# Optimization experiments

Measured on AMD Instinct MI355X. Metric: run time of the kernel, lower is better.

Reference implementation:

```python
import jax, jax.numpy as jnp
import numpy as np
from jax.scipy.stats import norm
from jax.scipy.special import ndtri

B, S, F = 512, 2048, 128

def setup_inputs() -> dict:
    key = jax.random.key(0)
    k1, k2, k3 = jax.random.split(key, 3)
    x = jax.random.normal(k1, (B, F), dtype=jnp.float32)
    cdf_data = jax.random.normal(k2, (S, F), dtype=jnp.float32)
    bw_param = jax.random.uniform(k3, (1, F), dtype=jnp.float32)
    return {"x": x, "cdf_data": cdf_data, "bw_param": bw_param}

def reference(x, cdf_data, bw_param):
    # trainable bandwidths: bw = sigmoid(raw param), shape [1, F]
    bw = jax.nn.sigmoid(bw_param)[0]  # [F]
    # Pairwise Gaussian-CDF KDE: for each (b, f), mean over stored samples s of
    # Phi((x[b,f] - cdf_data[s,f]) / bw[f]).  Intermediate z: [B, S, F].
    z = (x[:, None, :] - cdf_data[None, :, :]) / bw  # [B, S, F]
    u = jnp.mean(norm.cdf(z), axis=1)               # [B, F], uniform-ish in (0,1)
    # normal_backtransform=True: map uniform -> standard normal via inverse CDF
    return ndtri(u)
```

## Files before the change

kernel.cpp:

```cpp
#include <hip/hip_runtime.h>
#include <math.h>

#define FDIM  128
#define SDIM  2048
#define BDIM  512
#define GPTS  128
#define SP    8
#define PARTS 4
#define BLOCK1 (FDIM * PARTS)
#define XMIN  (-6.5)
#define XSPAN (13.0)

__device__ __forceinline__ double ndtri_pair(double u, double cu) {
    double q = u - 0.5;
    if (fabs(q) <= 0.425) {
        double r = 0.180625 - q * q;
        double num = (((((((2.5090809287301226727e3  * r + 3.3430575583588128105e4) * r +
                            6.7265770927008700853e4) * r + 4.5921953931549871457e4) * r +
                            1.3731693765509461125e4) * r + 1.9715909503065514427e3) * r +
                            1.3314166789178437745e2) * r + 3.3871328727963666080e0);
        double den = (((((((5.2264952788528545610e3  * r + 2.8729085735721942674e4) * r +
                            3.9307895800092710610e4) * r + 2.1213794301586595867e4) * r +
                            5.3941960214247511077e3) * r + 6.8718700749205790830e2) * r +
                            4.2313330701600911252e1) * r + 1.0);
        return q * num / den;
    }
    double r = (q < 0.0) ? u : cu;
    r = fmax(r, 1e-300);
    r = sqrt(-log(r));
    double val;
    if (r <= 5.0) {
        r -= 1.6;
        double num = (((((((7.74545014278341407640e-4 * r + 2.27238449892691845833e-2) * r +
                            2.41780725177450611770e-1) * r + 1.27045825245236838258e0) * r +
                            3.64784832476320460504e0)  * r + 5.76949722146069140550e0) * r +
                            4.63033784615654529590e0)  * r + 1.42343711074968357734e0);
        double den = (((((((1.05075007164441684324e-9 * r + 5.47593808499534494600e-4) * r +
                            1.51986665636164571966e-2) * r + 1.48103976427480074590e-1) * r +
                            6.89767334985100004550e-1) * r + 1.67638483018380384940e0) * r +
                            2.05319162663775882187e0)  * r + 1.0);
        val = num / den;
    } else {
        r -= 5.0;
        double num = (((((((2.01033439929228813265e-7 * r + 2.71155556874348757815e-5) * r +
                            1.24266094738807843860e-3) * r + 2.65321895265761230930e-2) * r +
                            2.96560571828504891230e-1) * r + 1.78482653991729133580e0) * r +
                            5.46378491116411436990e0)  * r + 6.65790464350110377720e0);
        double den = (((((((2.04426310338993978564e-15 * r + 1.42151175831644588870e-7) * r +
                            1.84631831751005468180e-5)  * r + 7.86869131145613259100e-4) * r +
                            1.48753612908506148525e-2)  * r + 1.36929880922735805310e-1) * r +
                            5.99832206555887937690e-1)  * r + 1.0);
        val = num / den;
    }
    return (q < 0.0) ? -val : val;
}

__device__ __forceinline__ float half_erfc_ex(float a, float& ex_out) {
    float t  = __builtin_amdgcn_rcpf(fmaf(0.3275911f, a, 1.0f));
    float ex = __expf(-a * a);
    ex_out = ex;
    float q  = fmaf(0.53070271450f, t, -0.72657601350f);
    q        = fmaf(q, t,  0.71070687050f);
    q        = fmaf(q, t, -0.14224836800f);
    q        = fmaf(q, t,  0.12741479600f);
    return q * t * ex;
}

__global__ __launch_bounds__(BLOCK1) void build_kernel(
    const float* __restrict__ cdf, const float* __restrict__ bwp,
    float* __restrict__ accP, float* __restrict__ dacP, int* __restrict__ npP)
{
    const int g    = blockIdx.x >> 3;
    const int sp   = blockIdx.x & (SP - 1);
    const int f    = threadIdx.x & (FDIM - 1);
    const int part = threadIdx.x >> 7;

    const float p = bwp[f];
    const float s = (1.0f + __expf(-p)) * 0.70710678118654752f;
    const float xg = (float)(XMIN + (double)g * (XSPAN / (GPTS - 1)));

    const int chunk = SDIM / SP / PARTS;
    const int base  = sp * (SDIM / SP) + part * chunk;
    const float* cp = cdf + base * FDIM + f;

    float acc0 = 0.f, acc1 = 0.f, acc2 = 0.f, acc3 = 0.f;
    float dac = 0.f;
    int npos = 0;

    for (int i = 0; i < chunk; i += 4) {
        float c0 = cp[0 * FDIM];
        float c1 = cp[1 * FDIM];
        float c2 = cp[2 * FDIM];
        float c3 = cp[3 * FDIM];
        cp += 4 * FDIM;

        float d0 = xg - c0, d1 = xg - c1, d2 = xg - c2, d3 = xg - c3;
        float x0, x1, x2, x3;
        float e0 = half_erfc_ex(fabsf(d0) * s, x0);
        float e1 = half_erfc_ex(fabsf(d1) * s, x1);
        float e2 = half_erfc_ex(fabsf(d2) * s, x2);
        float e3 = half_erfc_ex(fabsf(d3) * s, x3);

        bool p0 = d0 >= 0.f, p1 = d1 >= 0.f, p2 = d2 >= 0.f, p3 = d3 >= 0.f;
        acc0 += p0 ? -e0 : e0;
        acc1 += p1 ? -e1 : e1;
        acc2 += p2 ? -e2 : e2;
        acc3 += p3 ? -e3 : e3;
        npos += (int)p0 + (int)p1 + (int)p2 + (int)p3;
        dac  += (x0 + x1) + (x2 + x3);
    }

    __shared__ float sacc[PARTS][FDIM];
    __shared__ float sdac[PARTS][FDIM];
    __shared__ int   snp[PARTS][FDIM];
    sacc[part][f] = (acc0 + acc1) + (acc2 + acc3);
    sdac[part][f] = dac;
    snp[part][f]  = npos;
    __syncthreads();

    if (part == 0) {
        float a  = (sacc[0][f] + sacc[1][f]) + (sacc[2][f] + sacc[3][f]);
        float da = (sdac[0][f] + sdac[1][f]) + (sdac[2][f] + sdac[3][f]);
        int   np = snp[0][f] + snp[1][f] + snp[2][f] + snp[3][f];
        const int o = blockIdx.x * FDIM + f;
        accP[o] = a;
        dacP[o] = da;
        npP[o]  = np;
    }
}

__global__ __launch_bounds__(256) void table_kernel(
    const float* __restrict__ accP, const float* __restrict__ dacP,
    const int* __restrict__ npP, const float* __restrict__ bwp,
    double* __restrict__ Tu, double* __restrict__ Tcu, double* __restrict__ Td)
{
    const int idx = blockIdx.x * 256 + threadIdx.x;
    const int g = idx >> 7;
    const int f = idx & (FDIM - 1);
    (void)g;

    double a = 0.0, da = 0.0;
    int np = 0;
    #pragma unroll
    for (int sp = 0; sp < SP; ++sp) {
        const int o = ((idx >> 7) * SP + sp) * FDIM + f;
        a  += (double)accP[o];
        da += (double)dacP[o];
        np += npP[o];
    }
    const double invS = 1.0 / (double)SDIM;
    double u  = ((double)np + a) * invS;
    double cu = ((double)(SDIM - np) - a) * invS;
    double invbw = 1.0 + exp(-(double)bwp[f]);
    double du = da * invbw * (1.0 / ((double)SDIM * 2.5066282746310002));
    Tu[idx]  = u;
    Tcu[idx] = cu;
    Td[idx]  = du;
}

__global__ __launch_bounds__(256) void interp_kernel(
    const float* __restrict__ x,
    const double* __restrict__ Tu, const double* __restrict__ Tcu,
    const double* __restrict__ Td, float* __restrict__ out)
{
    const int idx = blockIdx.x * 256 + threadIdx.x;
    const int f = idx & (FDIM - 1);

    const double H = XSPAN / (GPTS - 1);
    double t = ((double)x[idx] - XMIN) * ((GPTS - 1) / XSPAN);
    t = fmin(fmax(t, 0.0), (double)(GPTS - 1));
    int i = (int)t;
    if (i > GPTS - 2) i = GPTS - 2;
    double w = t - (double)i;

    const int o0 = i * FDIM + f;
    const int o1 = o0 + FDIM;
    double u0 = Tu[o0],  u1 = Tu[o1];
    double c0 = Tcu[o0], c1 = Tcu[o1];
    double m0 = Td[o0],  m1 = Td[o1];

    double w2 = w * w, w3 = w2 * w;
    double h00 = 2.0 * w3 - 3.0 * w2 + 1.0;
    double h10 = w3 - 2.0 * w2 + w;
    double h01 = 3.0 * w2 - 2.0 * w3;
    double h11 = w3 - w2;
    double dterm = H * (h10 * m0 + h11 * m1);
    double u  = h00 * u0 + h01 * u1 + dterm;
    double cu = h00 * c0 + h01 * c1 - dterm;

    out[idx] = (float)ndtri_pair(u, cu);
}

extern "C" void kernel_launch(void* const* d_in, const int* in_sizes, int n_in,
                              void* d_out, int out_size, void* d_ws, size_t ws_size,
                              hipStream_t stream) {
    const float* x   = (const float*)d_in[0];
    const float* cdf = (const float*)d_in[1];
    const float* bwp = (const float*)d_in[2];
    float* out = (float*)d_out;

    const size_t GF   = (size_t)GPTS * FDIM;
    const size_t GSPF = (size_t)GPTS * SP * FDIM;
    char* wsb = (char*)d_ws;
    double* Tu   = (double*)wsb;
    double* Tcu  = Tu + GF;
    double* Td   = Tcu + GF;
    float*  accP = (float*)(Td + GF);
    float*  dacP = accP + GSPF;
    int*    npP  = (int*)(dacP + GSPF);

    build_kernel<<<dim3(GPTS * SP), dim3(BLOCK1), 0, stream>>>(cdf, bwp, accP, dacP, npP);
    table_kernel<<<dim3(GF / 256), dim3(256), 0, stream>>>(accP, dacP, npP, bwp, Tu, Tcu, Td);
    interp_kernel<<<dim3((BDIM * FDIM) / 256), dim3(256), 0, stream>>>(x, Tu, Tcu, Td, out);
}
```

Baseline: 80.37 us.

## Halve interpolation grid, fuse table reduction into interp kernel

Cuts the KDE grid from 128 to 64 points over a narrower range and doubles the sample splits per point, so build_kernel does half the erfc evaluations. It removes the separate table kernel by having interp_kernel reduce the 16 partial sums for the two bracketing grid points directly. It also adds an unroll hint to the build loop. The coarser grid and clipped range may reduce the accuracy of the Hermite interpolation, and the fused reduction does redundant gather work for each output element.

```diff
diff --git a/kernel.cpp b/kernel.cpp
--- a/kernel.cpp
+++ b/kernel.cpp
@@ -4,12 +4,12 @@
 #define FDIM  128
 #define SDIM  2048
 #define BDIM  512
-#define GPTS  128
-#define SP    8
+#define GPTS  64
+#define SP    16
 #define PARTS 4
 #define BLOCK1 (FDIM * PARTS)
-#define XMIN  (-6.5)
-#define XSPAN (13.0)
+#define XMIN  (-6.0)
+#define XSPAN (12.0)
 
 __device__ __forceinline__ double ndtri_pair(double u, double cu) {
     double q = u - 0.5;
@@ -70,7 +70,7 @@
     const float* __restrict__ cdf, const float* __restrict__ bwp,
     float* __restrict__ accP, float* __restrict__ dacP, int* __restrict__ npP)
 {
-    const int g    = blockIdx.x >> 3;
+    const int g    = blockIdx.x >> 4;
     const int sp   = blockIdx.x & (SP - 1);
     const int f    = threadIdx.x & (FDIM - 1);
     const int part = threadIdx.x >> 7;
@@ -87,6 +87,7 @@
     float dac = 0.f;
     int npos = 0;
 
+    #pragma unroll 2
     for (int i = 0; i < chunk; i += 4) {
         float c0 = cp[0 * FDIM];
         float c1 = cp[1 * FDIM];
@@ -129,56 +130,46 @@
     }
 }
 
-__global__ __launch_bounds__(256) void table_kernel(
+__global__ __launch_bounds__(256) void interp_kernel(
+    const float* __restrict__ x, const float* __restrict__ bwp,
     const float* __restrict__ accP, const float* __restrict__ dacP,
-    const int* __restrict__ npP, const float* __restrict__ bwp,
-    double* __restrict__ Tu, double* __restrict__ Tcu, double* __restrict__ Td)
-{
-    const int idx = blockIdx.x * 256 + threadIdx.x;
-    const int g = idx >> 7;
-    const int f = idx & (FDIM - 1);
-    (void)g;
-
-    double a = 0.0, da = 0.0;
-    int np = 0;
-    #pragma unroll
-    for (int sp = 0; sp < SP; ++sp) {
-        const int o = ((idx >> 7) * SP + sp) * FDIM + f;
-        a  += (double)accP[o];
-        da += (double)dacP[o];
-        np += npP[o];
-    }
-    const double invS = 1.0 / (double)SDIM;
-    double u  = ((double)np + a) * invS;
-    double cu = ((double)(SDIM - np) - a) * invS;
-    double invbw = 1.0 + exp(-(double)bwp[f]);
-    double du = da * invbw * (1.0 / ((double)SDIM * 2.5066282746310002));
-    Tu[idx]  = u;
-    Tcu[idx] = cu;
-    Td[idx]  = du;
-}
-
-__global__ __launch_bounds__(256) void interp_kernel(
-    const float* __restrict__ x,
-    const double* __restrict__ Tu, const double* __restrict__ Tcu,
-    const double* __restrict__ Td, float* __restrict__ out)
+    const int* __restrict__ npP, float* __restrict__ out)
 {
     const int idx = blockIdx.x * 256 + threadIdx.x;
     const int f = idx & (FDIM - 1);
 
-    const double H = XSPAN / (GPTS - 1);
     double t = ((double)x[idx] - XMIN) * ((GPTS - 1) / XSPAN);
     t = fmin(fmax(t, 0.0), (double)(GPTS - 1));
     int i = (int)t;
     if (i > GPTS - 2) i = GPTS - 2;
     double w = t - (double)i;
 
-    const int o0 = i * FDIM + f;
-    const int o1 = o0 + FDIM;
-    double u0 = Tu[o0],  u1 = Tu[o1];
-    double c0 = Tcu[o0], c1 = Tcu[o1];
-    double m0 = Td[o0],  m1 = Td[o1];
-
+    double a0 = 0.0, da0 = 0.0, a1 = 0.0, da1 = 0.0;
+    int np0 = 0, np1 = 0;
+    const float* pA = accP + (i * SP) * FDIM + f;
+    const float* pD = dacP + (i * SP) * FDIM + f;
+    const int*   pN = npP  + (i * SP) * FDIM + f;
+    #pragma unroll
+    for (int sp = 0; sp < SP; ++sp) {
+        a0  += (double)pA[sp * FDIM];
+        da0 += (double)pD[sp * FDIM];
+        np0 += pN[sp * FDIM];
+        a1  += (double)pA[(SP + sp) * FDIM];
+        da1 += (double)pD[(SP + sp) * FDIM];
+        np1 += pN[(SP + sp) * FDIM];
+    }
+
+    const double invS = 1.0 / (double)SDIM;
+    const double invbw = 1.0 + (double)__expf(-bwp[f]);
+    const double mscale = invbw * (invS / 2.5066282746310002);
+    double u0 = ((double)np0 + a0) * invS;
+    double cu0 = ((double)(SDIM - np0) - a0) * invS;
+    double m0 = da0 * mscale;
+    double u1 = ((double)np1 + a1) * invS;
+    double cu1 = ((double)(SDIM - np1) - a1) * invS;
+    double m1 = da1 * mscale;
+
+    const double H = XSPAN / (GPTS - 1);
     double w2 = w * w, w3 = w2 * w;
     double h00 = 2.0 * w3 - 3.0 * w2 + 1.0;
     double h10 = w3 - 2.0 * w2 + w;
@@ -186,7 +177,7 @@
     double h11 = w3 - w2;
     double dterm = H * (h10 * m0 + h11 * m1);
     double u  = h00 * u0 + h01 * u1 + dterm;
-    double cu = h00 * c0 + h01 * c1 - dterm;
+    double cu = h00 * cu0 + h01 * cu1 - dterm;
 
     out[idx] = (float)ndtri_pair(u, cu);
 }
@@ -199,17 +190,11 @@
     const float* bwp = (const float*)d_in[2];
     float* out = (float*)d_out;
 
-    const size_t GF   = (size_t)GPTS * FDIM;
     const size_t GSPF = (size_t)GPTS * SP * FDIM;
-    char* wsb = (char*)d_ws;
-    double* Tu   = (double*)wsb;
-    double* Tcu  = Tu + GF;
-    double* Td   = Tcu + GF;
-    float*  accP = (float*)(Td + GF);
-    float*  dacP = accP + GSPF;
-    int*    npP  = (int*)(dacP + GSPF);
+    float* accP = (float*)d_ws;
+    float* dacP = accP + GSPF;
+    int*   npP  = (int*)(dacP + GSPF);
 
     build_kernel<<<dim3(GPTS * SP), dim3(BLOCK1), 0, stream>>>(cdf, bwp, accP, dacP, npP);
-    table_kernel<<<dim3(GF / 256), dim3(256), 0, stream>>>(accP, dacP, npP, bwp, Tu, Tcu, Td);
-    interp_kernel<<<dim3((BDIM * FDIM) / 256), dim3(256), 0, stream>>>(x, Tu, Tcu, Td, out);
-}
+    interp_kernel<<<dim3((BDIM * FDIM) / 256), dim3(256), 0, stream>>>(x, bwp, accP, dacP, npP, out);
+}
```

Result: slower. 87.92 us (+9.4%).
